# Performance work log

Measured on AMD Instinct MI355X. Metric: run time of the kernel, lower is better.

## Reference

```python
import jax, jax.numpy as jnp
import numpy as np

H = 512

def setup_inputs() -> dict:
    key = jax.random.key(0)
    k1, k2, k3 = jax.random.split(key, 3)
    encoder_outputs = jax.random.normal(k1, (32, 4096, H), dtype=jnp.float32)  # (B,T,H)
    W = jax.random.normal(k2, (H, H), dtype=jnp.float32) * (1.0 / np.sqrt(H))  # attn.weight
    v = jax.random.normal(k3, (H,), dtype=jnp.float32) * (1.0 / np.sqrt(H))    # v param
    return {"encoder_outputs": encoder_outputs, "W": W, "v": v}

def reference(encoder_outputs, W, v):
    # score: energy = tanh(x @ W.T); attn_energies = v . energy over H -> (B,T)
    energy = jnp.tanh(jnp.einsum('bth,gh->btg', encoder_outputs, W))
    attn_energies = jnp.einsum('btg,g->bt', energy, v)
    # method == 'bmm': softmax over T, weighted sum over T -> (B,H)
    attn_w = jax.nn.softmax(attn_energies, axis=-1)
    out = jnp.einsum('bt,bth->bh', attn_w, encoder_outputs)
    return out
```

## Files before the change

### kernel.cpp

```cpp
#include <hip/hip_runtime.h>
#include <hip/hip_bf16.h>

typedef __attribute__((ext_vector_type(8))) short short8;
typedef __attribute__((ext_vector_type(4))) float f32x4;

#define B_SZ 32
#define T_SZ 4096
#define H_SZ 512
#define NROWS (B_SZ * T_SZ)

static __device__ __forceinline__ unsigned int pack2(float a, float b) {
  unsigned int r;
  asm("v_cvt_pk_bf16_f32 %0, %1, %2" : "=v"(r) : "v"(a), "v"(b));
  return r;
}
static __device__ __forceinline__ float fast_tanh(float x) {
  float e = __expf(2.0f * x);
  return 1.0f - 2.0f / (e + 1.0f);
}

__global__ __launch_bounds__(256) void prep_w_kernel(
    const float* __restrict__ W, uint4* __restrict__ Wfrag) {
  int s = blockIdx.x * 256 + threadIdx.x;
  int frow  = s & 15;
  int kslot = (s >> 4) & 3;
  int kt    = (s >> 6) & 15;
  int j     = (s >> 10) & 3;
  int c     = s >> 12;
  int g  = c * 64 + j * 16 + frow;
  int k0 = kt * 32 + kslot * 8;
  const float4* Wf4 = reinterpret_cast<const float4*>(W);
  float4 lo = Wf4[g * 128 + (k0 >> 2)];
  float4 hi = Wf4[g * 128 + (k0 >> 2) + 1];
  uint4 u;
  u.x = pack2(lo.x, lo.y); u.y = pack2(lo.z, lo.w);
  u.z = pack2(hi.x, hi.y); u.w = pack2(hi.z, hi.w);
  Wfrag[s] = u;
}

__global__ __launch_bounds__(256, 2) void score_fused_kernel(
    const float* __restrict__ X, const uint4* __restrict__ Wfrag,
    const float* __restrict__ v,
    float* __restrict__ num, float2* __restrict__ md) {
  __shared__ unsigned char WsB[65536];
  __shared__ float sLDS[128];
  __shared__ float pLDS[128];
  __shared__ float mred[2], dred[2];

  const int tid   = threadIdx.x;
  const int lane  = tid & 63;
  const int wave  = tid >> 6;
  const int frow  = lane & 15;
  const int kslot = lane >> 4;
  const size_t rowbase = (size_t)blockIdx.x * 128;

  short8 afrag0[16], afrag1[16];
  {
    const float4* xr0 = reinterpret_cast<const float4*>(X + (rowbase + wave * 32 + frow) * H_SZ);
    const float4* xr1 = reinterpret_cast<const float4*>(X + (rowbase + wave * 32 + 16 + frow) * H_SZ);
    #pragma unroll
    for (int kt = 0; kt < 16; ++kt) {
      float4 lo0 = xr0[kt * 8 + kslot * 2];
      float4 hi0 = xr0[kt * 8 + kslot * 2 + 1];
      union { uint4 u; short8 s; } c0;
      c0.u.x = pack2(lo0.x, lo0.y); c0.u.y = pack2(lo0.z, lo0.w);
      c0.u.z = pack2(hi0.x, hi0.y); c0.u.w = pack2(hi0.z, hi0.w);
      afrag0[kt] = c0.s;
      float4 lo1 = xr1[kt * 8 + kslot * 2];
      float4 hi1 = xr1[kt * 8 + kslot * 2 + 1];
      union { uint4 u; short8 s; } c1;
      c1.u.x = pack2(lo1.x, lo1.y); c1.u.y = pack2(lo1.z, lo1.w);
      c1.u.z = pack2(hi1.x, hi1.y); c1.u.w = pack2(hi1.z, hi1.w);
      afrag1[kt] = c1.s;
    }
  }

  float red0[4] = {0.f, 0.f, 0.f, 0.f};
  float red1[4] = {0.f, 0.f, 0.f, 0.f};

  for (int c = 0; c < 8; ++c) {
    {
      const char* src = (const char*)Wfrag + (size_t)c * 65536 + tid * 16;
      unsigned char* dst = WsB + tid * 16;
      #pragma unroll
      for (int i = 0; i < 16; ++i)
        __builtin_amdgcn_global_load_lds((const unsigned int*)(src + i * 4096),
                                         (unsigned int*)(dst + i * 4096), 16, 0, 0);
    }
    float vv0 = v[c * 64 + frow];
    float vv1 = v[c * 64 + 16 + frow];
    float vv2 = v[c * 64 + 32 + frow];
    float vv3 = v[c * 64 + 48 + frow];

    asm volatile("s_waitcnt vmcnt(0)" ::: "memory");
    __builtin_amdgcn_s_barrier();
    __builtin_amdgcn_sched_barrier(0);

    f32x4 acc[2][4];
    #pragma unroll
    for (int a = 0; a < 2; ++a)
      #pragma unroll
      for (int j = 0; j < 4; ++j)
        acc[a][j] = (f32x4){0.f, 0.f, 0.f, 0.f};

    const unsigned char* bb = WsB + lane * 16;
    __builtin_amdgcn_s_setprio(1);
    #pragma unroll
    for (int kt = 0; kt < 16; ++kt) {
      short8 b0 = *reinterpret_cast<const short8*>(bb + (0 * 16 + kt) * 1024);
      short8 b1 = *reinterpret_cast<const short8*>(bb + (1 * 16 + kt) * 1024);
      short8 b2 = *reinterpret_cast<const short8*>(bb + (2 * 16 + kt) * 1024);
      short8 b3 = *reinterpret_cast<const short8*>(bb + (3 * 16 + kt) * 1024);
      acc[0][0] = __builtin_amdgcn_mfma_f32_16x16x32_bf16(afrag0[kt], b0, acc[0][0], 0, 0, 0);
      acc[1][0] = __builtin_amdgcn_mfma_f32_16x16x32_bf16(afrag1[kt], b0, acc[1][0], 0, 0, 0);
      acc[0][1] = __builtin_amdgcn_mfma_f32_16x16x32_bf16(afrag0[kt], b1, acc[0][1], 0, 0, 0);
      acc[1][1] = __builtin_amdgcn_mfma_f32_16x16x32_bf16(afrag1[kt], b1, acc[1][1], 0, 0, 0);
      acc[0][2] = __builtin_amdgcn_mfma_f32_16x16x32_bf16(afrag0[kt], b2, acc[0][2], 0, 0, 0);
      acc[1][2] = __builtin_amdgcn_mfma_f32_16x16x32_bf16(afrag1[kt], b2, acc[1][2], 0, 0, 0);
      acc[0][3] = __builtin_amdgcn_mfma_f32_16x16x32_bf16(afrag0[kt], b3, acc[0][3], 0, 0, 0);
      acc[1][3] = __builtin_amdgcn_mfma_f32_16x16x32_bf16(afrag1[kt], b3, acc[1][3], 0, 0, 0);
    }
    __builtin_amdgcn_s_setprio(0);

    #pragma unroll
    for (int r = 0; r < 4; ++r) {
      red0[r] = fmaf(vv0, fast_tanh(acc[0][0][r]), red0[r]);
      red0[r] = fmaf(vv1, fast_tanh(acc[0][1][r]), red0[r]);
      red0[r] = fmaf(vv2, fast_tanh(acc[0][2][r]), red0[r]);
      red0[r] = fmaf(vv3, fast_tanh(acc[0][3][r]), red0[r]);
      red1[r] = fmaf(vv0, fast_tanh(acc[1][0][r]), red1[r]);
      red1[r] = fmaf(vv1, fast_tanh(acc[1][1][r]), red1[r]);
      red1[r] = fmaf(vv2, fast_tanh(acc[1][2][r]), red1[r]);
      red1[r] = fmaf(vv3, fast_tanh(acc[1][3][r]), red1[r]);
    }

    __builtin_amdgcn_s_barrier();
  }

  #pragma unroll
  for (int r = 0; r < 4; ++r) {
    #pragma unroll
    for (int d = 1; d < 16; d <<= 1) {
      red0[r] += __shfl_xor(red0[r], d);
      red1[r] += __shfl_xor(red1[r], d);
    }
  }
  if (frow == 0) {
    float* sp = sLDS + wave * 32 + kslot * 4;
    sp[0]  = red0[0]; sp[1]  = red0[1]; sp[2]  = red0[2]; sp[3]  = red0[3];
    sp[16] = red1[0]; sp[17] = red1[1]; sp[18] = red1[2]; sp[19] = red1[3];
  }
  __syncthreads();

  if (tid < 128) {
    float s = sLDS[tid];
    float m = s;
    #pragma unroll
    for (int d = 1; d < 64; d <<= 1) m = fmaxf(m, __shfl_xor(m, d));
    if ((tid & 63) == 0) mred[tid >> 6] = m;
  }
  __syncthreads();
  const float m_loc = fmaxf(mred[0], mred[1]);
  if (tid < 128) {
    float p = __expf(sLDS[tid] - m_loc);
    pLDS[tid] = p;
    #pragma unroll
    for (int d = 1; d < 64; d <<= 1) p += __shfl_xor(p, d);
    if ((tid & 63) == 0) dred[tid >> 6] = p;
  }
  __syncthreads();

  {
    float ax = 0.f, ay = 0.f;
    const float2* xb = reinterpret_cast<const float2*>(X + rowbase * H_SZ) + tid;
    #pragma unroll 8
    for (int t = 0; t < 128; ++t) {
      float p = pLDS[t];
      float2 xv = xb[(size_t)t * (H_SZ / 2)];
      ax = fmaf(p, xv.x, ax);
      ay = fmaf(p, xv.y, ay);
    }
    float2 r; r.x = ax; r.y = ay;
    reinterpret_cast<float2*>(num + (size_t)blockIdx.x * H_SZ)[tid] = r;
  }
  if (tid == 0) {
    float2 r; r.x = m_loc; r.y = dred[0] + dred[1];
    md[blockIdx.x] = r;
  }
}

__global__ __launch_bounds__(512) void combine_kernel(
    const float* __restrict__ num, const float2* __restrict__ md,
    float* __restrict__ out) {
  const int b = blockIdx.x;
  const int h = threadIdx.x;
  float M = -1e30f;
  #pragma unroll
  for (int c = 0; c < 32; ++c) M = fmaxf(M, md[b * 32 + c].x);
  float den = 0.f, acc = 0.f;
  #pragma unroll 4
  for (int c = 0; c < 32; ++c) {
    float2 m2 = md[b * 32 + c];
    float w = __expf(m2.x - M);
    den += w * m2.y;
    acc = fmaf(w, num[(size_t)(b * 32 + c) * H_SZ + h], acc);
  }
  out[b * H_SZ + h] = acc / den;
}

extern "C" void kernel_launch(void* const* d_in, const int* in_sizes, int n_in,
                              void* d_out, int out_size, void* d_ws, size_t ws_size,
                              hipStream_t stream) {
  const float* X = (const float*)d_in[0];
  const float* W = (const float*)d_in[1];
  const float* v = (const float*)d_in[2];
  float* out = (float*)d_out;
  unsigned char* ws = (unsigned char*)d_ws;

  uint4* Wfrag = (uint4*)(ws);
  float* num   = (float*)(ws + (512u << 10));
  float2* md   = (float2*)(ws + (512u << 10) + (2u << 20));

  prep_w_kernel<<<128, 256, 0, stream>>>(W, Wfrag);
  score_fused_kernel<<<NROWS / 128, 256, 0, stream>>>(X, Wfrag, v, num, md);
  combine_kernel<<<B_SZ, 512, 0, stream>>>(num, md, out);
}
```

Measured before the change: 138.6 us.

## Switch score GEMM from 16x16x32 to 32x32x16 MFMA tiles

Reworks the W fragment layout, the X fragment loads and the score loop so each wave computes a 32-row by 64-column tile with 32x32x16 bf16 MFMAs. Alternating k-steps accumulate into separate accumulators to break the dependency chain, and the pairs are summed before the tanh. The larger tiles cut LDS B-fragment reads and the instruction count per FLOP. In exchange each lane holds 64 accumulator registers, and the shuffle reduction now spans 32 lanes with a new row-index mapping.

```diff
diff --git a/kernel.cpp b/kernel.cpp
--- a/kernel.cpp
+++ b/kernel.cpp
@@ -1,8 +1,8 @@
 #include <hip/hip_runtime.h>
 #include <hip/hip_bf16.h>
 
-typedef __attribute__((ext_vector_type(8))) short short8;
-typedef __attribute__((ext_vector_type(4))) float f32x4;
+typedef __attribute__((ext_vector_type(8)))  short short8;
+typedef __attribute__((ext_vector_type(16))) float f32x16;
 
 #define B_SZ 32
 #define T_SZ 4096
@@ -22,13 +22,12 @@
 __global__ __launch_bounds__(256) void prep_w_kernel(
     const float* __restrict__ W, uint4* __restrict__ Wfrag) {
   int s = blockIdx.x * 256 + threadIdx.x;
-  int frow  = s & 15;
-  int kslot = (s >> 4) & 3;
-  int kt    = (s >> 6) & 15;
-  int j     = (s >> 10) & 3;
-  int c     = s >> 12;
-  int g  = c * 64 + j * 16 + frow;
-  int k0 = kt * 32 + kslot * 8;
+  int lane = s & 63;
+  int kt   = (s >> 6) & 31;
+  int j    = (s >> 11) & 1;
+  int c    = s >> 12;
+  int g  = c * 64 + j * 32 + (lane & 31);
+  int k0 = kt * 16 + (lane >> 5) * 8;
   const float4* Wf4 = reinterpret_cast<const float4*>(W);
   float4 lo = Wf4[g * 128 + (k0 >> 2)];
   float4 hi = Wf4[g * 128 + (k0 >> 2) + 1];
@@ -50,33 +49,28 @@
   const int tid   = threadIdx.x;
   const int lane  = tid & 63;
   const int wave  = tid >> 6;
-  const int frow  = lane & 15;
-  const int kslot = lane >> 4;
+  const int l31   = lane & 31;
+  const int half  = lane >> 5;
   const size_t rowbase = (size_t)blockIdx.x * 128;
 
-  short8 afrag0[16], afrag1[16];
+  short8 afrag[32];
   {
-    const float4* xr0 = reinterpret_cast<const float4*>(X + (rowbase + wave * 32 + frow) * H_SZ);
-    const float4* xr1 = reinterpret_cast<const float4*>(X + (rowbase + wave * 32 + 16 + frow) * H_SZ);
-    #pragma unroll
-    for (int kt = 0; kt < 16; ++kt) {
-      float4 lo0 = xr0[kt * 8 + kslot * 2];
-      float4 hi0 = xr0[kt * 8 + kslot * 2 + 1];
-      union { uint4 u; short8 s; } c0;
-      c0.u.x = pack2(lo0.x, lo0.y); c0.u.y = pack2(lo0.z, lo0.w);
-      c0.u.z = pack2(hi0.x, hi0.y); c0.u.w = pack2(hi0.z, hi0.w);
-      afrag0[kt] = c0.s;
-      float4 lo1 = xr1[kt * 8 + kslot * 2];
-      float4 hi1 = xr1[kt * 8 + kslot * 2 + 1];
-      union { uint4 u; short8 s; } c1;
-      c1.u.x = pack2(lo1.x, lo1.y); c1.u.y = pack2(lo1.z, lo1.w);
-      c1.u.z = pack2(hi1.x, hi1.y); c1.u.w = pack2(hi1.z, hi1.w);
-      afrag1[kt] = c1.s;
-    }
-  }
-
-  float red0[4] = {0.f, 0.f, 0.f, 0.f};
-  float red1[4] = {0.f, 0.f, 0.f, 0.f};
+    const float4* xr = reinterpret_cast<const float4*>(
+        X + (rowbase + wave * 32 + l31) * H_SZ);
+    #pragma unroll
+    for (int kt = 0; kt < 32; ++kt) {
+      float4 lo = xr[kt * 4 + half * 2];
+      float4 hi = xr[kt * 4 + half * 2 + 1];
+      union { uint4 u; short8 s; } cv;
+      cv.u.x = pack2(lo.x, lo.y); cv.u.y = pack2(lo.z, lo.w);
+      cv.u.z = pack2(hi.x, hi.y); cv.u.w = pack2(hi.z, hi.w);
+      afrag[kt] = cv.s;
+    }
+  }
+
+  float red[16];
+  #pragma unroll
+  for (int r = 0; r < 16; ++r) red[r] = 0.f;
 
   for (int c = 0; c < 8; ++c) {
     {
@@ -87,68 +81,51 @@
         __builtin_amdgcn_global_load_lds((const unsigned int*)(src + i * 4096),
                                          (unsigned int*)(dst + i * 4096), 16, 0, 0);
     }
-    float vv0 = v[c * 64 + frow];
-    float vv1 = v[c * 64 + 16 + frow];
-    float vv2 = v[c * 64 + 32 + frow];
-    float vv3 = v[c * 64 + 48 + frow];
+    float vv0 = v[c * 64 + l31];
+    float vv1 = v[c * 64 + 32 + l31];
 
     asm volatile("s_waitcnt vmcnt(0)" ::: "memory");
     __builtin_amdgcn_s_barrier();
     __builtin_amdgcn_sched_barrier(0);
 
-    f32x4 acc[2][4];
-    #pragma unroll
-    for (int a = 0; a < 2; ++a)
-      #pragma unroll
-      for (int j = 0; j < 4; ++j)
-        acc[a][j] = (f32x4){0.f, 0.f, 0.f, 0.f};
+    f32x16 acc00 = {0}, acc01 = {0}, acc10 = {0}, acc11 = {0};
 
     const unsigned char* bb = WsB + lane * 16;
     __builtin_amdgcn_s_setprio(1);
     #pragma unroll
-    for (int kt = 0; kt < 16; ++kt) {
-      short8 b0 = *reinterpret_cast<const short8*>(bb + (0 * 16 + kt) * 1024);
-      short8 b1 = *reinterpret_cast<const short8*>(bb + (1 * 16 + kt) * 1024);
-      short8 b2 = *reinterpret_cast<const short8*>(bb + (2 * 16 + kt) * 1024);
-      short8 b3 = *reinterpret_cast<const short8*>(bb + (3 * 16 + kt) * 1024);
-      acc[0][0] = __builtin_amdgcn_mfma_f32_16x16x32_bf16(afrag0[kt], b0, acc[0][0], 0, 0, 0);
-      acc[1][0] = __builtin_amdgcn_mfma_f32_16x16x32_bf16(afrag1[kt], b0, acc[1][0], 0, 0, 0);
-      acc[0][1] = __builtin_amdgcn_mfma_f32_16x16x32_bf16(afrag0[kt], b1, acc[0][1], 0, 0, 0);
-      acc[1][1] = __builtin_amdgcn_mfma_f32_16x16x32_bf16(afrag1[kt], b1, acc[1][1], 0, 0, 0);
-      acc[0][2] = __builtin_amdgcn_mfma_f32_16x16x32_bf16(afrag0[kt], b2, acc[0][2], 0, 0, 0);
-      acc[1][2] = __builtin_amdgcn_mfma_f32_16x16x32_bf16(afrag1[kt], b2, acc[1][2], 0, 0, 0);
-      acc[0][3] = __builtin_amdgcn_mfma_f32_16x16x32_bf16(afrag0[kt], b3, acc[0][3], 0, 0, 0);
-      acc[1][3] = __builtin_amdgcn_mfma_f32_16x16x32_bf16(afrag1[kt], b3, acc[1][3], 0, 0, 0);
+    for (int kt = 0; kt < 32; kt += 2) {
+      short8 b0a = *reinterpret_cast<const short8*>(bb + (kt)     * 1024);
+      short8 b0b = *reinterpret_cast<const short8*>(bb + (kt + 1) * 1024);
+      short8 b1a = *reinterpret_cast<const short8*>(bb + 32768 + (kt)     * 1024);
+      short8 b1b = *reinterpret_cast<const short8*>(bb + 32768 + (kt + 1) * 1024);
+      acc00 = __builtin_amdgcn_mfma_f32_32x32x16_bf16(afrag[kt],     b0a, acc00, 0, 0, 0);
+      acc10 = __builtin_amdgcn_mfma_f32_32x32x16_bf16(afrag[kt],     b1a, acc10, 0, 0, 0);
+      acc01 = __builtin_amdgcn_mfma_f32_32x32x16_bf16(afrag[kt + 1], b0b, acc01, 0, 0, 0);
+      acc11 = __builtin_amdgcn_mfma_f32_32x32x16_bf16(afrag[kt + 1], b1b, acc11, 0, 0, 0);
     }
     __builtin_amdgcn_s_setprio(0);
 
     #pragma unroll
-    for (int r = 0; r < 4; ++r) {
-      red0[r] = fmaf(vv0, fast_tanh(acc[0][0][r]), red0[r]);
-      red0[r] = fmaf(vv1, fast_tanh(acc[0][1][r]), red0[r]);
-      red0[r] = fmaf(vv2, fast_tanh(acc[0][2][r]), red0[r]);
-      red0[r] = fmaf(vv3, fast_tanh(acc[0][3][r]), red0[r]);
-      red1[r] = fmaf(vv0, fast_tanh(acc[1][0][r]), red1[r]);
-      red1[r] = fmaf(vv1, fast_tanh(acc[1][1][r]), red1[r]);
-      red1[r] = fmaf(vv2, fast_tanh(acc[1][2][r]), red1[r]);
-      red1[r] = fmaf(vv3, fast_tanh(acc[1][3][r]), red1[r]);
+    for (int r = 0; r < 16; ++r) {
+      red[r] = fmaf(vv0, fast_tanh(acc00[r] + acc01[r]), red[r]);
+      red[r] = fmaf(vv1, fast_tanh(acc10[r] + acc11[r]), red[r]);
     }
 
     __builtin_amdgcn_s_barrier();
   }
 
   #pragma unroll
-  for (int r = 0; r < 4; ++r) {
-    #pragma unroll
-    for (int d = 1; d < 16; d <<= 1) {
-      red0[r] += __shfl_xor(red0[r], d);
-      red1[r] += __shfl_xor(red1[r], d);
-    }
-  }
-  if (frow == 0) {
-    float* sp = sLDS + wave * 32 + kslot * 4;
-    sp[0]  = red0[0]; sp[1]  = red0[1]; sp[2]  = red0[2]; sp[3]  = red0[3];
-    sp[16] = red1[0]; sp[17] = red1[1]; sp[18] = red1[2]; sp[19] = red1[3];
+  for (int r = 0; r < 16; ++r) {
+    #pragma unroll
+    for (int d = 1; d < 32; d <<= 1)
+      red[r] += __shfl_xor(red[r], d);
+  }
+  if (l31 == 0) {
+    #pragma unroll
+    for (int r = 0; r < 16; ++r) {
+      int row = (r & 3) + 8 * (r >> 2) + 4 * half;
+      sLDS[wave * 32 + row] = red[r];
+    }
   }
   __syncthreads();
 
```

New measurement: 141.1 us. Within noise of the previous version (+1.8%).

## Double-buffer W fragment chunks in LDS and prefetch during compute

Applied to the files above, without the earlier changes.

W is now split into 16 chunks of 32 output columns instead of 8 chunks of 64, held in two 32 KB LDS buffers. Chunk ch+2 is loaded asynchronously while chunk ch is being computed, so the per-chunk global-to-LDS wait no longer stalls the MFMA work. The first two chunks are issued before the X fragment loads so they overlap with them. The v vector is staged once into LDS rather than re-read from global memory in every chunk. The cost is twice as many barrier/wait points, and fewer MFMAs between them, which may limit how much latency actually gets hidden.

```diff
diff --git a/kernel.cpp b/kernel.cpp
--- a/kernel.cpp
+++ b/kernel.cpp
@@ -25,9 +25,9 @@
   int frow  = s & 15;
   int kslot = (s >> 4) & 3;
   int kt    = (s >> 6) & 15;
-  int j     = (s >> 10) & 3;
-  int c     = s >> 12;
-  int g  = c * 64 + j * 16 + frow;
+  int j     = (s >> 10) & 1;
+  int c     = s >> 11;
+  int g  = c * 32 + j * 16 + frow;
   int k0 = kt * 32 + kslot * 8;
   const float4* Wf4 = reinterpret_cast<const float4*>(W);
   float4 lo = Wf4[g * 128 + (k0 >> 2)];
@@ -42,7 +42,8 @@
     const float* __restrict__ X, const uint4* __restrict__ Wfrag,
     const float* __restrict__ v,
     float* __restrict__ num, float2* __restrict__ md) {
-  __shared__ unsigned char WsB[65536];
+  __shared__ unsigned char WsB[2][32768];
+  __shared__ float vLDS[512];
   __shared__ float sLDS[128];
   __shared__ float pLDS[128];
   __shared__ float mred[2], dred[2];
@@ -53,6 +54,20 @@
   const int frow  = lane & 15;
   const int kslot = lane >> 4;
   const size_t rowbase = (size_t)blockIdx.x * 128;
+
+  #define STAGE(c, buf)                                                         \
+    {                                                                           \
+      const char* src = (const char*)Wfrag + (size_t)(c) * 32768 + tid * 16;    \
+      unsigned char* dst = &WsB[buf][tid * 16];                                 \
+      _Pragma("unroll")                                                         \
+      for (int i = 0; i < 8; ++i)                                               \
+        __builtin_amdgcn_global_load_lds((const unsigned int*)(src + i * 4096), \
+                                         (unsigned int*)(dst + i * 4096), 16, 0, 0); \
+    }
+
+  STAGE(0, 0);
+  STAGE(1, 1);
+  reinterpret_cast<float2*>(vLDS)[tid] = reinterpret_cast<const float2*>(v)[tid];
 
   short8 afrag0[16], afrag1[16];
   {
@@ -74,51 +89,35 @@
       afrag1[kt] = c1.s;
     }
   }
+  asm volatile("s_waitcnt vmcnt(0) lgkmcnt(0)" ::: "memory");
+  __builtin_amdgcn_s_barrier();
+  __builtin_amdgcn_sched_barrier(0);
 
   float red0[4] = {0.f, 0.f, 0.f, 0.f};
   float red1[4] = {0.f, 0.f, 0.f, 0.f};
 
-  for (int c = 0; c < 8; ++c) {
-    {
-      const char* src = (const char*)Wfrag + (size_t)c * 65536 + tid * 16;
-      unsigned char* dst = WsB + tid * 16;
-      #pragma unroll
-      for (int i = 0; i < 16; ++i)
-        __builtin_amdgcn_global_load_lds((const unsigned int*)(src + i * 4096),
-                                         (unsigned int*)(dst + i * 4096), 16, 0, 0);
-    }
-    float vv0 = v[c * 64 + frow];
-    float vv1 = v[c * 64 + 16 + frow];
-    float vv2 = v[c * 64 + 32 + frow];
-    float vv3 = v[c * 64 + 48 + frow];
-
-    asm volatile("s_waitcnt vmcnt(0)" ::: "memory");
-    __builtin_amdgcn_s_barrier();
-    __builtin_amdgcn_sched_barrier(0);
-
-    f32x4 acc[2][4];
+  for (int ch = 0; ch < 16; ++ch) {
+    const int buf = ch & 1;
+    float vv0 = vLDS[ch * 32 + frow];
+    float vv1 = vLDS[ch * 32 + 16 + frow];
+
+    f32x4 acc[2][2];
     #pragma unroll
     for (int a = 0; a < 2; ++a)
       #pragma unroll
-      for (int j = 0; j < 4; ++j)
+      for (int j = 0; j < 2; ++j)
         acc[a][j] = (f32x4){0.f, 0.f, 0.f, 0.f};
 
-    const unsigned char* bb = WsB + lane * 16;
+    const unsigned char* bb = &WsB[buf][lane * 16];
     __builtin_amdgcn_s_setprio(1);
     #pragma unroll
     for (int kt = 0; kt < 16; ++kt) {
-      short8 b0 = *reinterpret_cast<const short8*>(bb + (0 * 16 + kt) * 1024);
-      short8 b1 = *reinterpret_cast<const short8*>(bb + (1 * 16 + kt) * 1024);
-      short8 b2 = *reinterpret_cast<const short8*>(bb + (2 * 16 + kt) * 1024);
-      short8 b3 = *reinterpret_cast<const short8*>(bb + (3 * 16 + kt) * 1024);
+      short8 b0 = *reinterpret_cast<const short8*>(bb + kt * 1024);
+      short8 b1 = *reinterpret_cast<const short8*>(bb + 16384 + kt * 1024);
       acc[0][0] = __builtin_amdgcn_mfma_f32_16x16x32_bf16(afrag0[kt], b0, acc[0][0], 0, 0, 0);
       acc[1][0] = __builtin_amdgcn_mfma_f32_16x16x32_bf16(afrag1[kt], b0, acc[1][0], 0, 0, 0);
       acc[0][1] = __builtin_amdgcn_mfma_f32_16x16x32_bf16(afrag0[kt], b1, acc[0][1], 0, 0, 0);
       acc[1][1] = __builtin_amdgcn_mfma_f32_16x16x32_bf16(afrag1[kt], b1, acc[1][1], 0, 0, 0);
-      acc[0][2] = __builtin_amdgcn_mfma_f32_16x16x32_bf16(afrag0[kt], b2, acc[0][2], 0, 0, 0);
-      acc[1][2] = __builtin_amdgcn_mfma_f32_16x16x32_bf16(afrag1[kt], b2, acc[1][2], 0, 0, 0);
-      acc[0][3] = __builtin_amdgcn_mfma_f32_16x16x32_bf16(afrag0[kt], b3, acc[0][3], 0, 0, 0);
-      acc[1][3] = __builtin_amdgcn_mfma_f32_16x16x32_bf16(afrag1[kt], b3, acc[1][3], 0, 0, 0);
     }
     __builtin_amdgcn_s_setprio(0);
 
@@ -126,16 +125,16 @@
     for (int r = 0; r < 4; ++r) {
       red0[r] = fmaf(vv0, fast_tanh(acc[0][0][r]), red0[r]);
       red0[r] = fmaf(vv1, fast_tanh(acc[0][1][r]), red0[r]);
-      red0[r] = fmaf(vv2, fast_tanh(acc[0][2][r]), red0[r]);
-      red0[r] = fmaf(vv3, fast_tanh(acc[0][3][r]), red0[r]);
       red1[r] = fmaf(vv0, fast_tanh(acc[1][0][r]), red1[r]);
       red1[r] = fmaf(vv1, fast_tanh(acc[1][1][r]), red1[r]);
-      red1[r] = fmaf(vv2, fast_tanh(acc[1][2][r]), red1[r]);
-      red1[r] = fmaf(vv3, fast_tanh(acc[1][3][r]), red1[r]);
-    }
-
+    }
+
+    asm volatile("s_waitcnt vmcnt(0)" ::: "memory");
     __builtin_amdgcn_s_barrier();
-  }
+    __builtin_amdgcn_sched_barrier(0);
+    if (ch + 2 < 16) STAGE(ch + 2, buf);
+  }
+  #undef STAGE
 
   #pragma unroll
   for (int r = 0; r < 4; ++r) {
```

Result: faster. 135.7 us (median of 2 runs) (-2.0%).
